# Optimization experiments

Hardware: AMD Instinct MI355X
Metric: run time of the kernel (lower is better)

The kernel has to match this reference:

```python
import jax, jax.numpy as jnp
import numpy as np
import math

STEP_SIZE = 1.0


def setup_inputs() -> dict:
    key = jax.random.key(0)
    ks = jax.random.split(key, 6)
    B, L, C, H, O = 4096, 256, 8, 128, 1
    n_int = L - 1
    coeffs = jax.random.normal(ks[0], (B, n_int, 4 * C), dtype=jnp.float32) * 0.1

    def lin(k, i, o):
        kw, kb = jax.random.split(k)
        s = 1.0 / math.sqrt(i)
        W = jax.random.uniform(kw, (i, o), minval=-s, maxval=s, dtype=jnp.float32)
        b = jax.random.uniform(kb, (o,), minval=-s, maxval=s, dtype=jnp.float32)
        return W, b

    W_init, b_init = lin(ks[1], C, H)
    W1, b1 = lin(ks[2], H, H)
    W2, b2 = lin(ks[3], H, H)
    W3, b3 = lin(ks[4], H, H * C)
    W_out, b_out = lin(ks[5], H, O)
    return dict(coeffs=coeffs, W_init=W_init, b_init=b_init, W1=W1, b1=b1,
                W2=W2, b2=b2, W3=W3, b3=b3, W_out=W_out, b_out=b_out)


def reference(coeffs, W_init, b_init, W1, b1, W2, b2, W3, b3, W_out, b_out):
    B, n_int, four_c = coeffs.shape
    C = four_c // 4
    H = W1.shape[0]
    # torchcde CubicSpline coefficient layout: a, b, two_c, three_d
    a, bcoef, two_c, three_d = jnp.split(coeffs, 4, axis=-1)  # each (B, n_int, C)
    knots = jnp.arange(n_int + 1, dtype=coeffs.dtype)  # t = linspace(0, n_int, n_int+1)
    T = float(n_int)

    def X_deriv(t):
        # torchcde _interpret_t: bucketize(t, knots)-1 clamped; here knots uniform
        idx = jnp.clip(jnp.searchsorted(knots, t, side='left') - 1, 0, n_int - 1)
        frac = t - knots[idx]
        return bcoef[:, idx] + (two_c[:, idx] + three_d[:, idx] * frac) * frac  # (B, C)

    def ode_f(t, z):
        # CDEFunc: Linear->Softplus x2, Linear->Tanh, reshape to (B, H, C)
        h = jax.nn.softplus(z @ W1 + b1)
        h = jax.nn.softplus(h @ W2 + b2)
        f = jnp.tanh(h @ W3 + b3).reshape(B, H, C)
        return jnp.einsum('bhc,bc->bh', f, X_deriv(t))  # f(z) @ dX/dt

    # torchdiffeq fixed-grid rk4 with step_size (3/8 rule: rk4_alt_step_func)
    n_steps = int(math.ceil(T / STEP_SIZE))
    ts = jnp.minimum(jnp.arange(n_steps + 1, dtype=coeffs.dtype) * STEP_SIZE, T)
    t0s, dts = ts[:-1], ts[1:] - ts[:-1]

    z0 = a[:, 0] @ W_init + b_init  # X.evaluate(interval[0]) == a at first knot

    def step(z, td):
        t0, dt = td
        k1 = ode_f(t0, z)
        k2 = ode_f(t0 + dt / 3, z + dt * k1 / 3)
        k3 = ode_f(t0 + dt * 2 / 3, z + dt * (k2 - k1 / 3))
        k4 = ode_f(t0 + dt, z + dt * (k1 - k2 + k3))
        return z + dt * (k1 + 3.0 * (k2 + k3) + k4) / 8.0, None

    zT, _ = jax.lax.scan(step, z0, (t0s, dts))
    return zT @ W_out + b_out
```

## Files before the change

kernel.cpp:

```cpp
#include <hip/hip_runtime.h>

#define NINT  255
#define BM    16
#define PITCH 136

typedef __bf16 bf16x8 __attribute__((ext_vector_type(8)));
typedef float  f32x4  __attribute__((ext_vector_type(4)));

#define MFMA(a, b, c) __builtin_amdgcn_mfma_f32_16x16x32_bf16((a), (b), (c), 0, 0, 0)

__device__ __forceinline__ unsigned short f2b(float f) {
    __bf16 b = (__bf16)f;
    return __builtin_bit_cast(unsigned short, b);
}

__device__ __forceinline__ float sp_f(float x) {
    float e = __builtin_amdgcn_exp2f(x * 1.4426950408889634f);
    float y = __builtin_amdgcn_logf(1.0f + e) * 0.6931471805599453f;
    return (x > 80.0f) ? x : y;
}

__device__ __forceinline__ float tanh_f(float x) {
    float e = __builtin_amdgcn_exp2f(x * 2.8853900817779268f);
    float r = __builtin_amdgcn_rcpf(e + 1.0f);
    return fmaf(-2.0f, r, 1.0f);
}

__global__ void prep_frags(const float* __restrict__ W1, const float* __restrict__ W2,
                           const float* __restrict__ W3,
                           unsigned short* __restrict__ W1f, unsigned short* __restrict__ W2f,
                           unsigned short* __restrict__ W3f) {
    const int e = blockIdx.x * 256 + threadIdx.x;
    const int i = e & 7;
    const int l = (e >> 3) & 63;
    const int t = (e >> 9) & 3;
    const int n = e >> 11;
    const int k = 32 * t + ((l >> 4) & 3) * 8 + i;
    const int c = l & 15;
    if (e < 16384) {
        W1f[e] = f2b(W1[k * 128 + 16 * n + c]);
        W2f[e] = f2b(W2[k * 128 + 16 * n + c]);
    }
    W3f[e] = f2b(W3[k * 1024 + 16 * n + c]);
}

#define RK_UPDATE(ST, JL, HOFF)                                                  \
{                                                                                \
    float znew;                                                                  \
    if (ST == 0)      { k1r[JL] = p; znew = zb[JL] + p * (1.0f/3.0f); }          \
    else if (ST == 1) { k2r[JL] = p; znew = zb[JL] + p - k1r[JL] * (1.0f/3.0f); }\
    else if (ST == 2) { k3r[JL] = p; znew = zb[JL] + k1r[JL] - k2r[JL] + p; }    \
    else { zb[JL] = fmaf(k1r[JL] + 3.0f*(k2r[JL] + k3r[JL]) + p, 0.125f, zb[JL]); znew = zb[JL]; } \
    if ((g & 1) == 0)                                                            \
        Zs[l15 * PITCH + (HOFF) + h2wb] = f2b(znew);                             \
}

#define STAGE_BODY(ST)                                                           \
{                                                                                \
    if (w < 8) {                                                                 \
        bf16x8 a0[4];                                                            \
        _Pragma("unroll") for (int t = 0; t < 4; ++t)                            \
            a0[t] = *(const bf16x8*)(Zs + l15 * PITCH + t * 32 + koff);          \
        f32x4 h1 = {b1r, b1r, b1r, b1r};                                         \
        _Pragma("unroll") for (int t = 0; t < 4; ++t)                            \
            h1 = MFMA(a0[t], wf1[(w * 4 + t) * 64 + l], h1);                     \
        _Pragma("unroll") for (int i = 0; i < 4; ++i)                            \
            H1s[(g * 4 + i) * PITCH + 16 * w + l15] = f2b(sp_f(h1[i]));          \
    }                                                                            \
    __syncthreads();                                                             \
    if (w < 8) {                                                                 \
        bf16x8 a1[4];                                                            \
        _Pragma("unroll") for (int t = 0; t < 4; ++t)                            \
            a1[t] = *(const bf16x8*)(H1s + l15 * PITCH + t * 32 + koff);         \
        f32x4 h2 = {b2r, b2r, b2r, b2r};                                         \
        _Pragma("unroll") for (int t = 0; t < 4; ++t)                            \
            h2 = MFMA(a1[t], wf2[(w * 4 + t) * 64 + l], h2);                     \
        _Pragma("unroll") for (int i = 0; i < 4; ++i)                            \
            H2s[(g * 4 + i) * PITCH + 16 * w + l15] = f2b(sp_f(h2[i]));          \
    }                                                                            \
    __syncthreads();                                                             \
    {                                                                            \
        bf16x8 bfr[4];                                                           \
        _Pragma("unroll") for (int t = 0; t < 4; ++t)                            \
            bfr[t] = *(const bf16x8*)(H2s + l15 * PITCH + t * 32 + koff);        \
        f32x4 xdv;                                                               \
        if (ST == 0) xdv = xd0;                                                  \
        else if (ST == 1) { _Pragma("unroll") for (int i = 0; i < 4; ++i)        \
            xdv[i] = bB[i] + (tcv[i] + tdv[i] * (1.0f/3.0f)) * (1.0f/3.0f); }    \
        else if (ST == 2) { _Pragma("unroll") for (int i = 0; i < 4; ++i)        \
            xdv[i] = bB[i] + (tcv[i] + tdv[i] * (2.0f/3.0f)) * (2.0f/3.0f); }    \
        else { _Pragma("unroll") for (int i = 0; i < 4; ++i)                     \
            xdv[i] = bB[i] + tcv[i] + tdv[i];  xd0 = xdv; }                      \
                              \
        {                                                                        \
            f32x4 acc0 = *(const f32x4*)&b3s[16 * (w) + 4 * g];                  \
            f32x4 acc1 = *(const f32x4*)&b3s[16 * (16 + w) + 4 * g];             \
            _Pragma("unroll") for (int t = 0; t < 4; ++t) {                      \
                acc0 = MFMA(w3g[0][t], bfr[t], acc0);                            \
                acc1 = MFMA(w3g[1][t], bfr[t], acc1);                            \
            }                                                                    \
            float p;                                                             \
            p = 0.0f;                                                            \
            _Pragma("unroll") for (int i = 0; i < 4; ++i)                        \
                p = fmaf(tanh_f(acc0[i]), xdv[i], p);                            \
            p += __shfl_xor(p, 16, 64);                                          \
            RK_UPDATE(ST, 0, 0)                                                  \
            p = 0.0f;                                                            \
            _Pragma("unroll") for (int i = 0; i < 4; ++i)                        \
                p = fmaf(tanh_f(acc1[i]), xdv[i], p);                            \
            p += __shfl_xor(p, 16, 64);                                          \
            RK_UPDATE(ST, 1, 32)                                                 \
        }                                                                        \
                              \
        {                                                                        \
            f32x4 acc0 = *(const f32x4*)&b3s[16 * (32 + w) + 4 * g];             \
            f32x4 acc1 = *(const f32x4*)&b3s[16 * (48 + w) + 4 * g];             \
            _Pragma("unroll") for (int t = 0; t < 4; ++t) {                      \
                acc0 = MFMA(w3g[2][t], bfr[t], acc0);                            \
                acc1 = MFMA(w3lv[(w * 4 + t) * 64 + l], bfr[t], acc1);           \
            }                                                                    \
            float p;                                                             \
            p = 0.0f;                                                            \
            _Pragma("unroll") for (int i = 0; i < 4; ++i)                        \
                p = fmaf(tanh_f(acc0[i]), xdv[i], p);                            \
            p += __shfl_xor(p, 16, 64);                                          \
            RK_UPDATE(ST, 2, 64)                                                 \
            p = 0.0f;                                                            \
            _Pragma("unroll") for (int i = 0; i < 4; ++i)                        \
                p = fmaf(tanh_f(acc1[i]), xdv[i], p);                            \
            p += __shfl_xor(p, 16, 64);                                          \
            RK_UPDATE(ST, 3, 96)                                                 \
        }                                                                        \
    }                                                                            \
    __syncthreads();                                                             \
}

__global__ __launch_bounds__(1024, 4)
void cde_mfma(const float* __restrict__ coeffs,
              const float* __restrict__ W_init, const float* __restrict__ b_init,
              const float* __restrict__ b1, const float* __restrict__ b2,
              const float* __restrict__ b3,
              const float* __restrict__ W_out, const float* __restrict__ b_out,
              const unsigned short* __restrict__ w1f, const unsigned short* __restrict__ w2f,
              const unsigned short* __restrict__ w3f,
              float* __restrict__ out)
{
    __shared__ __align__(16) unsigned short W1f_lds[16384];
    __shared__ __align__(16) unsigned short W2f_lds[16384];
    __shared__ __align__(16) unsigned short W3l_lds[32768];
    __shared__ __align__(16) unsigned short Zs [BM * PITCH];
    __shared__ __align__(16) unsigned short H1s[BM * PITCH];
    __shared__ __align__(16) unsigned short H2s[BM * PITCH];
    __shared__ __align__(16) float b3s[1024];
    __shared__ __align__(16) float Outp[32][16];

    const int tid     = threadIdx.x;
    const int rowbase = blockIdx.x * BM;
    const int l       = tid & 63;
    const int w       = tid >> 6;
    const int l15     = l & 15;
    const int g       = (l >> 4) & 3;
    const int hb      = g >> 1;
    const int chB     = 4 * (g & 1);
    const int koff    = g * 8;
    const int h2wb    = 2 * w + hb;

    for (int k4 = tid; k4 < 2048; k4 += 1024) {
        ((uint4*)W1f_lds)[k4] = ((const uint4*)w1f)[k4];
        ((uint4*)W2f_lds)[k4] = ((const uint4*)w2f)[k4];
    }
    for (int k4 = tid; k4 < 4096; k4 += 1024)
        ((uint4*)W3l_lds)[k4] = ((const uint4*)(w3f + 48 * 2048))[k4];
    b3s[tid & 1023] = b3[tid & 1023];

    const bf16x8* w3v = (const bf16x8*)w3f;
    bf16x8 w3g[3][4];
    #pragma unroll
    for (int jl = 0; jl < 3; ++jl)
        #pragma unroll
        for (int t = 0; t < 4; ++t)
            w3g[jl][t] = w3v[((16 * jl + w) * 4 + t) * 64 + l];

    const float b1r = b1[16 * (w & 7) + l15];
    const float b2r = b2[16 * (w & 7) + l15];

    float zb[4], k1r[4], k2r[4], k3r[4];
    {
        const float* ap = coeffs + (size_t)(rowbase + l15) * (NINT * 32);
        float av[8];
        #pragma unroll
        for (int c = 0; c < 8; ++c) av[c] = ap[c];
        #pragma unroll
        for (int jl = 0; jl < 4; ++jl) {
            const int h = 32 * jl + h2wb;
            float z = b_init[h];
            #pragma unroll
            for (int c = 0; c < 8; ++c) z = fmaf(av[c], W_init[c * 128 + h], z);
            zb[jl] = z;
            if ((g & 1) == 0) Zs[l15 * PITCH + h] = f2b(z);
        }
    }

    const float* cpx = coeffs + (size_t)(rowbase + l15) * (NINT * 32) + chB;
    f32x4 bB, tcv, tdv;
    f32x4 xd0 = *(const f32x4*)(cpx + 8);

    const bf16x8* wf1  = (const bf16x8*)W1f_lds;
    const bf16x8* wf2  = (const bf16x8*)W2f_lds;
    const bf16x8* w3lv = (const bf16x8*)W3l_lds;
    __syncthreads();

    #pragma unroll 1
    for (int step = 0; step < NINT; ++step) {
        const float* cc = cpx + step * 32;
        bB  = *(const f32x4*)(cc + 8);
        tcv = *(const f32x4*)(cc + 16);
        tdv = *(const f32x4*)(cc + 24);

        STAGE_BODY(0)
        STAGE_BODY(1)
        STAGE_BODY(2)
        STAGE_BODY(3)
    }

    if ((g & 1) == 0) {
        float prt = 0.0f;
        #pragma unroll
        for (int jl = 0; jl < 4; ++jl)
            prt = fmaf(zb[jl], W_out[32 * jl + h2wb], prt);
        Outp[h2wb][l15] = prt;
    }
    __syncthreads();
    if (tid < 16) {
        float s = b_out[0];
        #pragma unroll
        for (int p = 0; p < 32; ++p) s += Outp[p][tid];
        out[rowbase + tid] = s;
    }
}

extern "C" void kernel_launch(void* const* d_in, const int* in_sizes, int n_in,
                              void* d_out, int out_size, void* d_ws, size_t ws_size,
                              hipStream_t stream) {
    const float* coeffs = (const float*)d_in[0];
    const float* W_init = (const float*)d_in[1];
    const float* b_init = (const float*)d_in[2];
    const float* W1     = (const float*)d_in[3];
    const float* b1     = (const float*)d_in[4];
    const float* W2     = (const float*)d_in[5];
    const float* b2     = (const float*)d_in[6];
    const float* W3     = (const float*)d_in[7];
    const float* b3     = (const float*)d_in[8];
    const float* W_out  = (const float*)d_in[9];
    const float* b_out  = (const float*)d_in[10];
    float* outp = (float*)d_out;

    unsigned short* w1f = (unsigned short*)d_ws;
    unsigned short* w2f = w1f + 16384;
    unsigned short* w3f = w2f + 16384;

    hipLaunchKernelGGL(prep_frags, dim3(512), dim3(256), 0, stream, W1, W2, W3, w1f, w2f, w3f);
    hipLaunchKernelGGL(cde_mfma, dim3(4096 / BM), dim3(1024), 0, stream,
                       coeffs, W_init, b_init, b1, b2, b3, W_out, b_out,
                       w1f, w2f, w3f, outp);
}
```

Before: 3.000 ms.

## Stream W1/W2 fragments from global into rotating registers, move more W3 into LDS

Drops the W1 and W2 fragment copies from LDS. Each wave now holds one set of W1/W2 fragments in registers and reloads the other layer's fragments from global memory (expected to hit cache) right after issuing its MFMAs. The freed LDS holds half of W3 instead of a quarter, so one fewer W3 group stays resident in registers. This trades LDS reads for global/L2 loads on the critical path, which may add latency in exchange for lower register pressure and higher LDS residency.

```diff
diff --git a/kernel.cpp b/kernel.cpp
--- a/kernel.cpp
+++ b/kernel.cpp
@@ -44,7 +44,7 @@
     W3f[e] = f2b(W3[k * 1024 + 16 * n + c]);
 }
 
-#define RK_UPDATE(ST, JL, HOFF)                                                  \
+#define RK_UPDATE(ST, JL)                                                        \
 {                                                                                \
     float znew;                                                                  \
     if (ST == 0)      { k1r[JL] = p; znew = zb[JL] + p * (1.0f/3.0f); }          \
@@ -52,7 +52,7 @@
     else if (ST == 2) { k3r[JL] = p; znew = zb[JL] + k1r[JL] - k2r[JL] + p; }    \
     else { zb[JL] = fmaf(k1r[JL] + 3.0f*(k2r[JL] + k3r[JL]) + p, 0.125f, zb[JL]); znew = zb[JL]; } \
     if ((g & 1) == 0)                                                            \
-        Zs[l15 * PITCH + (HOFF) + h2wb] = f2b(znew);                             \
+        Zs[l15 * PITCH + 32 * JL + h2wb] = f2b(znew);                            \
 }
 
 #define STAGE_BODY(ST)                                                           \
@@ -63,7 +63,9 @@
             a0[t] = *(const bf16x8*)(Zs + l15 * PITCH + t * 32 + koff);          \
         f32x4 h1 = {b1r, b1r, b1r, b1r};                                         \
         _Pragma("unroll") for (int t = 0; t < 4; ++t)                            \
-            h1 = MFMA(a0[t], wf1[(w * 4 + t) * 64 + l], h1);                     \
+            h1 = MFMA(a0[t], w12r[t], h1);                                       \
+        _Pragma("unroll") for (int t = 0; t < 4; ++t)                            \
+            w12r[t] = w2v[(w * 4 + t) * 64 + l];               \
         _Pragma("unroll") for (int i = 0; i < 4; ++i)                            \
             H1s[(g * 4 + i) * PITCH + 16 * w + l15] = f2b(sp_f(h1[i]));          \
     }                                                                            \
@@ -74,7 +76,9 @@
             a1[t] = *(const bf16x8*)(H1s + l15 * PITCH + t * 32 + koff);         \
         f32x4 h2 = {b2r, b2r, b2r, b2r};                                         \
         _Pragma("unroll") for (int t = 0; t < 4; ++t)                            \
-            h2 = MFMA(a1[t], wf2[(w * 4 + t) * 64 + l], h2);                     \
+            h2 = MFMA(a1[t], w12r[t], h2);                                       \
+        _Pragma("unroll") for (int t = 0; t < 4; ++t)                            \
+            w12r[t] = w1v[(w * 4 + t) * 64 + l];            \
         _Pragma("unroll") for (int i = 0; i < 4; ++i)                            \
             H2s[(g * 4 + i) * PITCH + 16 * w + l15] = f2b(sp_f(h2[i]));          \
     }                                                                            \
@@ -91,9 +95,9 @@
             xdv[i] = bB[i] + (tcv[i] + tdv[i] * (2.0f/3.0f)) * (2.0f/3.0f); }    \
         else { _Pragma("unroll") for (int i = 0; i < 4; ++i)                     \
             xdv[i] = bB[i] + tcv[i] + tdv[i];  xd0 = xdv; }                      \
-                              \
+                                           \
         {                                                                        \
-            f32x4 acc0 = *(const f32x4*)&b3s[16 * (w) + 4 * g];                  \
+            f32x4 acc0 = *(const f32x4*)&b3s[16 * w + 4 * g];                    \
             f32x4 acc1 = *(const f32x4*)&b3s[16 * (16 + w) + 4 * g];             \
             _Pragma("unroll") for (int t = 0; t < 4; ++t) {                      \
                 acc0 = MFMA(w3g[0][t], bfr[t], acc0);                            \
@@ -104,32 +108,32 @@
             _Pragma("unroll") for (int i = 0; i < 4; ++i)                        \
                 p = fmaf(tanh_f(acc0[i]), xdv[i], p);                            \
             p += __shfl_xor(p, 16, 64);                                          \
-            RK_UPDATE(ST, 0, 0)                                                  \
+            RK_UPDATE(ST, 0)                                                     \
             p = 0.0f;                                                            \
             _Pragma("unroll") for (int i = 0; i < 4; ++i)                        \
                 p = fmaf(tanh_f(acc1[i]), xdv[i], p);                            \
             p += __shfl_xor(p, 16, 64);                                          \
-            RK_UPDATE(ST, 1, 32)                                                 \
+            RK_UPDATE(ST, 1)                                                     \
         }                                                                        \
-                              \
+                     \
         {                                                                        \
             f32x4 acc0 = *(const f32x4*)&b3s[16 * (32 + w) + 4 * g];             \
             f32x4 acc1 = *(const f32x4*)&b3s[16 * (48 + w) + 4 * g];             \
             _Pragma("unroll") for (int t = 0; t < 4; ++t) {                      \
-                acc0 = MFMA(w3g[2][t], bfr[t], acc0);                            \
-                acc1 = MFMA(w3lv[(w * 4 + t) * 64 + l], bfr[t], acc1);           \
+                acc0 = MFMA(w3lv[(w * 4 + t) * 64 + l], bfr[t], acc0);           \
+                acc1 = MFMA(w3lv[((16 + w) * 4 + t) * 64 + l], bfr[t], acc1);    \
             }                                                                    \
             float p;                                                             \
             p = 0.0f;                                                            \
             _Pragma("unroll") for (int i = 0; i < 4; ++i)                        \
                 p = fmaf(tanh_f(acc0[i]), xdv[i], p);                            \
             p += __shfl_xor(p, 16, 64);                                          \
-            RK_UPDATE(ST, 2, 64)                                                 \
+            RK_UPDATE(ST, 2)                                                     \
             p = 0.0f;                                                            \
             _Pragma("unroll") for (int i = 0; i < 4; ++i)                        \
                 p = fmaf(tanh_f(acc1[i]), xdv[i], p);                            \
             p += __shfl_xor(p, 16, 64);                                          \
-            RK_UPDATE(ST, 3, 96)                                                 \
+            RK_UPDATE(ST, 3)                                                     \
         }                                                                        \
     }                                                                            \
     __syncthreads();                                                             \
@@ -145,9 +149,7 @@
               const unsigned short* __restrict__ w3f,
               float* __restrict__ out)
 {
-    __shared__ __align__(16) unsigned short W1f_lds[16384];
-    __shared__ __align__(16) unsigned short W2f_lds[16384];
-    __shared__ __align__(16) unsigned short W3l_lds[32768];
+    __shared__ __align__(16) unsigned short W3l_lds[65536];
     __shared__ __align__(16) unsigned short Zs [BM * PITCH];
     __shared__ __align__(16) unsigned short H1s[BM * PITCH];
     __shared__ __align__(16) unsigned short H2s[BM * PITCH];
@@ -161,28 +163,33 @@
     const int l15     = l & 15;
     const int g       = (l >> 4) & 3;
     const int hb      = g >> 1;
+    const int koff    = g * 8;
     const int chB     = 4 * (g & 1);
-    const int koff    = g * 8;
     const int h2wb    = 2 * w + hb;
 
-    for (int k4 = tid; k4 < 2048; k4 += 1024) {
-        ((uint4*)W1f_lds)[k4] = ((const uint4*)w1f)[k4];
-        ((uint4*)W2f_lds)[k4] = ((const uint4*)w2f)[k4];
-    }
-    for (int k4 = tid; k4 < 4096; k4 += 1024)
-        ((uint4*)W3l_lds)[k4] = ((const uint4*)(w3f + 48 * 2048))[k4];
-    b3s[tid & 1023] = b3[tid & 1023];
-
+    for (int k4 = tid; k4 < 8192; k4 += 1024)
+        ((uint4*)W3l_lds)[k4] = ((const uint4*)(w3f + 32 * 2048))[k4];
+    b3s[tid] = b3[tid];
+
+    const bf16x8* w1v = (const bf16x8*)w1f;
+    const bf16x8* w2v = (const bf16x8*)w2f;
     const bf16x8* w3v = (const bf16x8*)w3f;
-    bf16x8 w3g[3][4];
+    bf16x8 w3g[2][4];
     #pragma unroll
-    for (int jl = 0; jl < 3; ++jl)
+    for (int jl = 0; jl < 2; ++jl)
         #pragma unroll
         for (int t = 0; t < 4; ++t)
             w3g[jl][t] = w3v[((16 * jl + w) * 4 + t) * 64 + l];
 
-    const float b1r = b1[16 * (w & 7) + l15];
-    const float b2r = b2[16 * (w & 7) + l15];
+    bf16x8 w12r[4];
+    float b1r = 0.0f, b2r = 0.0f;
+    if (w < 8) {
+        #pragma unroll
+        for (int t = 0; t < 4; ++t)
+            w12r[t] = w1v[(w * 4 + t) * 64 + l];
+        b1r = b1[16 * w + l15];
+        b2r = b2[16 * w + l15];
+    }
 
     float zb[4], k1r[4], k2r[4], k3r[4];
     {
@@ -205,8 +212,6 @@
     f32x4 bB, tcv, tdv;
     f32x4 xd0 = *(const f32x4*)(cpx + 8);
 
-    const bf16x8* wf1  = (const bf16x8*)W1f_lds;
-    const bf16x8* wf2  = (const bf16x8*)W2f_lds;
     const bf16x8* w3lv = (const bf16x8*)W3l_lds;
     __syncthreads();
 
```

New measurement: 3.393 ms. 13.1% more time.
